# Performance work log

Hardware: AMD Instinct MI355X
Metric: run time of the kernel (lower is better)

## Reference

```python
import jax, jax.numpy as jnp
from jax import lax
import numpy as np

B, T, D = 8, 2048, 1024
EPS = 1e-8


def zc_rms(x, g):
    x0 = x - jnp.mean(x, axis=-1, keepdims=True)
    return x0 * jax.lax.rsqrt(jnp.mean(x0 * x0, axis=-1, keepdims=True) + EPS) * g


def l2norm(x):
    return x * jax.lax.rsqrt(jnp.sum(x * x, axis=-1, keepdims=True) + EPS)


def dwconv3(x, w, b):
    # x: [B, T, D]; w: [D, 3] depthwise kernel; b: [D]
    xc = jnp.transpose(x, (0, 2, 1))  # [B, D, T]
    y = lax.conv_general_dilated(xc, w[:, None, :], window_strides=(1,),
                                 padding=[(1, 1)],
                                 dimension_numbers=('NCH', 'OIH', 'NCH'),
                                 feature_group_count=w.shape[0])
    return jnp.transpose(y + b[:, None], (0, 2, 1))  # [B, T, D]


def setup_inputs() -> dict:
    key = jax.random.key(0)
    ks = jax.random.split(key, 16)
    s = 1.0 / np.sqrt(D)
    inp = {
        'x': jax.random.normal(ks[0], (B, T, D), jnp.float32),
        'g1': jnp.ones((D,), jnp.float32),
        'Wq': jax.random.normal(ks[1], (D, D), jnp.float32) * s,
        'bq': jnp.zeros((D,), jnp.float32),
        'Wk': jax.random.normal(ks[2], (D, D), jnp.float32) * s,
        'bk': jnp.zeros((D,), jnp.float32),
        'Wv': jax.random.normal(ks[3], (D, D), jnp.float32) * s,
        'bv': jnp.zeros((D,), jnp.float32),
        'wqc': jax.random.normal(ks[4], (D, 3), jnp.float32) * 0.5,
        'bqc': jnp.zeros((D,), jnp.float32),
        'wkc': jax.random.normal(ks[5], (D, 3), jnp.float32) * 0.5,
        'bkc': jnp.zeros((D,), jnp.float32),
        'wvc': jax.random.normal(ks[6], (D, 3), jnp.float32) * 0.5,
        'bvc': jnp.zeros((D,), jnp.float32),
        'Wa': jax.random.normal(ks[7], (D, D), jnp.float32) * s,
        'ba': jnp.zeros((D,), jnp.float32),
        'Wb': jax.random.normal(ks[8], (D, D), jnp.float32) * s,
        'bb': jnp.zeros((D,), jnp.float32),
        'g2': jnp.ones((D,), jnp.float32),
        'Wp': jax.random.normal(ks[9], (D, D), jnp.float32) * s,
        'bp': jnp.zeros((D,), jnp.float32),
    }
    return inp


def reference(x, g1, Wq, bq, Wk, bk, Wv, bv, wqc, bqc, wkc, bkc, wvc, bvc,
              Wa, ba, Wb, bb, g2, Wp, bp):
    h = zc_rms(x, g1)
    q = jax.nn.sigmoid(dwconv3(h @ Wq + bq, wqc, bqc))
    k = jax.nn.sigmoid(dwconv3(h @ Wk + bk, wkc, bkc))
    v = jax.nn.sigmoid(dwconv3(h @ Wv + bv, wvc, bvc))
    q, k = l2norm(q), l2norm(k)
    delta = q * (k * v)
    delta = jnp.tanh(x @ Wa + ba) * delta + (x @ Wb + bb)
    dhat = zc_rms(delta, g2) @ Wp + bp
    # dropout is identity in eval mode
    return x + jax.nn.sigmoid(jax.nn.silu(dhat)) * dhat
```

## Files before the change

kernel.cpp:

```cpp
#include <hip/hip_runtime.h>
#include <stdint.h>

#define DD 1024
#define TT 2048
#define BBATCH 8
#define MM (BBATCH*TT)

typedef unsigned short u16;
typedef unsigned int   u32;

typedef __attribute__((ext_vector_type(8))) __bf16 bf16x8;
typedef __attribute__((ext_vector_type(4))) float  floatx4;
typedef __attribute__((ext_vector_type(4))) unsigned short u16x4;
typedef __attribute__((ext_vector_type(8))) unsigned short u16x8;
typedef __attribute__((ext_vector_type(4))) unsigned int   u32x4;

__device__ __forceinline__ float b2f(u16 v){
    u32 x = ((u32)v) << 16;
    return __builtin_bit_cast(float, x);
}
__device__ __forceinline__ u16 f2b(float f){
    u32 u = __builtin_bit_cast(u32, f);
    u32 r = (u + 0x7fffu + ((u >> 16) & 1u)) >> 16;
    return (u16)r;
}
__device__ __forceinline__ float sigf(float x){
    return 1.0f / (1.0f + __expf(-x));
}
__device__ __forceinline__ float tanhfast(float x){
    float e = __expf(2.0f * x);
    return 1.0f - 2.0f / (e + 1.0f);
}

__device__ __forceinline__ void g2l16(const u16* g, u16* l){
    __builtin_amdgcn_global_load_lds(
        (const __attribute__((address_space(1))) u32*)g,
        (__attribute__((address_space(3))) u32*)l, 16, 0, 0);
}

__device__ __forceinline__ u32 lds_u32(const u16* p){
    return (u32)(size_t)(const __attribute__((address_space(3))) u16*)p;
}

template<int OFF>
__device__ __forceinline__ bf16x8 dsr(u32 addr){
    u32x4 d;
    asm volatile("ds_read_b128 %0, %1 offset:%2" : "=v"(d) : "v"(addr), "i"(OFF));
    return __builtin_bit_cast(bf16x8, d);
}

template<int BASE>
__device__ __forceinline__ void rd_a8(bf16x8 (&arr)[8], u32 a0, u32 a1){
    arr[0]=dsr<BASE+0>(a0);    arr[1]=dsr<BASE+0>(a1);
    arr[2]=dsr<BASE+2048>(a0); arr[3]=dsr<BASE+2048>(a1);
    arr[4]=dsr<BASE+4096>(a0); arr[5]=dsr<BASE+4096>(a1);
    arr[6]=dsr<BASE+6144>(a0); arr[7]=dsr<BASE+6144>(a1);
}
template<int BASE>
__device__ __forceinline__ void rd_b4(bf16x8 (&arr)[4], u32 a0, u32 a1){
    arr[0]=dsr<BASE+0>(a0);    arr[1]=dsr<BASE+0>(a1);
    arr[2]=dsr<BASE+2048>(a0); arr[3]=dsr<BASE+2048>(a1);
}

__device__ __forceinline__ void load4bf(const u16* p, float* o){
    u16x4 v = *(const u16x4*)p;
    o[0] = b2f(v.x); o[1] = b2f(v.y); o[2] = b2f(v.z); o[3] = b2f(v.w);
}

__device__ __forceinline__ void wave_reduce2(float& a, float& b){
    #pragma unroll
    for (int m = 32; m; m >>= 1){
        a += __shfl_xor(a, m, 64);
        b += __shfl_xor(b, m, 64);
    }
}

__device__ __forceinline__ void block_reduce2(float& a, float& b, float* red, int tid){
    #pragma unroll
    for (int off = 32; off; off >>= 1){
        a += __shfl_down(a, off, 64);
        b += __shfl_down(b, off, 64);
    }
    __syncthreads();
    if ((tid & 63) == 0){ red[tid >> 6] = a; red[4 + (tid >> 6)] = b; }
    __syncthreads();
    a = red[0] + red[1] + red[2] + red[3];
    b = red[4] + red[5] + red[6] + red[7];
}

__global__ __launch_bounds__(256) void transpose_w(
    const float* __restrict__ s0, const float* __restrict__ s1, const float* __restrict__ s2,
    const float* __restrict__ s3, const float* __restrict__ s4, const float* __restrict__ s5,
    u16* __restrict__ dst_base)
{
    __shared__ u16 tile[32][33];
    const float* srcs[6] = {s0, s1, s2, s3, s4, s5};
    const int z = blockIdx.z;
    const float* src = srcs[z];
    u16* dst = dst_base + (size_t)z * (DD * (size_t)DD);
    const int tx = threadIdx.x, ty = threadIdx.y;
    const int x = blockIdx.x * 32 + tx;
    #pragma unroll
    for (int i = 0; i < 4; i++){
        int y = blockIdx.y * 32 + ty + i * 8;
        tile[ty + i * 8][tx] = f2b(src[(size_t)y * DD + x]);
    }
    __syncthreads();
    const int x2 = blockIdx.y * 32 + tx;
    #pragma unroll
    for (int i = 0; i < 4; i++){
        int y2 = blockIdx.x * 32 + ty + i * 8;
        dst[(size_t)y2 * DD + x2] = tile[tx][ty + i * 8];
    }
}

__global__ __launch_bounds__(256) void prep_wc(
    const float* __restrict__ w0, const float* __restrict__ w1, const float* __restrict__ w2,
    float* __restrict__ wcT)
{
    const float* srcs[3] = {w0, w1, w2};
    const int s = blockIdx.x / 3, tap = blockIdx.x % 3;
    #pragma unroll
    for (int i = 0; i < 4; i++){
        int d = threadIdx.x + i * 256;
        wcT[(s * 3 + tap) * DD + d] = srcs[s][d * 3 + tap];
    }
}

__global__ __launch_bounds__(256) void prep_rows(
    const float* __restrict__ in, const float* __restrict__ g,
    u16* __restrict__ xb, u16* __restrict__ h)
{
    const int tid = threadIdx.x;
    const int w = tid >> 6, lane = tid & 63;
    const int row = blockIdx.x * 4 + w;
    const int d0 = lane * 16;
    const size_t base = (size_t)row * DD + d0;

    float v[16];
    #pragma unroll
    for (int c = 0; c < 4; c++){
        floatx4 t = *(const floatx4*)(in + base + c * 4);
        v[c*4+0] = t.x; v[c*4+1] = t.y; v[c*4+2] = t.z; v[c*4+3] = t.w;
    }
    u16x8 x0, x1;
    #pragma unroll
    for (int j = 0; j < 8; j++){ x0[j] = f2b(v[j]); x1[j] = f2b(v[8+j]); }
    *(u16x8*)(xb + base)     = x0;
    *(u16x8*)(xb + base + 8) = x1;

    float s1 = 0.f, s2 = 0.f;
    #pragma unroll
    for (int j = 0; j < 16; j++){ s1 += v[j]; s2 += v[j]*v[j]; }
    wave_reduce2(s1, s2);
    const float mu = s1 * (1.0f / DD);
    const float ms = fmaxf(s2 * (1.0f / DD) - mu * mu, 0.0f);
    const float sc = rsqrtf(ms + 1e-8f);

    u16x8 o0, o1;
    #pragma unroll
    for (int j = 0; j < 8; j++)  o0[j] = f2b((v[j]     - mu) * sc * g[d0 + j]);
    #pragma unroll
    for (int j = 0; j < 8; j++)  o1[j] = f2b((v[8 + j] - mu) * sc * g[d0 + 8 + j]);
    *(u16x8*)(h + base)     = o0;
    *(u16x8*)(h + base + 8) = o1;
}

struct GemmPtrs {
    const u16*   A[5];
    const u16*   W[5];
    const float* bias[5];
    u16*         out[5];
};

#define BAR()   asm volatile("s_barrier" ::: "memory")
#define LGKM0() asm volatile("s_waitcnt lgkmcnt(0)" ::: "memory")
#define VM4()   asm volatile("s_waitcnt vmcnt(4)" ::: "memory")
#define SB0()   __builtin_amdgcn_sched_barrier(0)
#define PRIO1() __builtin_amdgcn_s_setprio(1)
#define PRIO0() __builtin_amdgcn_s_setprio(0)

template<int IH, int JH>
__device__ __forceinline__ void mm8(floatx4 (&acc)[8][4], const bf16x8 (&af)[8], const bf16x8 (&bf)[4]){
    #pragma unroll
    for (int kk = 0; kk < 2; kk++)
        #pragma unroll
        for (int i = 0; i < 4; i++)
            #pragma unroll
            for (int j = 0; j < 2; j++)
                acc[IH*4+i][JH*2+j] = __builtin_amdgcn_mfma_f32_16x16x32_bf16(
                    af[i*2+kk], bf[j*2+kk], acc[IH*4+i][JH*2+j], 0, 0, 0);
}

template<int MODE>
__global__ __launch_bounds__(512, 2) void gemm_bf16(
    GemmPtrs ptrs, const float* __restrict__ xres, float* __restrict__ dout)
{
    __shared__ alignas(16) u16 lds[65536];

    const int z = blockIdx.z;
    const u16*   __restrict__ A    = ptrs.A[z];
    const u16*   __restrict__ W    = ptrs.W[z];
    const float* __restrict__ bias = ptrs.bias[z];
    u16* __restrict__ Cout = ptrs.out[z];

    const int tid  = threadIdx.x;
    const int wave = tid >> 6, lane = tid & 63;
    const int quad = lane >> 4, l16 = lane & 15;
    const int wrow = wave >> 2, wcol = wave & 3;
    const int bm = blockIdx.x * 256;
    const int bn = blockIdx.y * 256;

    const int coloff = (((tid & 7) ^ ((tid >> 3) & 7)) * 8);
    const u16* srcA = A + (size_t)(bm + (tid >> 3)) * DD + coloff;
    const u16* srcB = W + (size_t)(bn + (tid >> 3)) * DD + coloff;

    #define STAGE_A(T,H) do{ \
        u16* _d = &lds[(((T)&1)*2 + (H))*8192 + tid*8]; \
        const u16* _g = srcA + (size_t)(H)*128*DD + (size_t)(((T)&15)*64); \
        g2l16(_g, _d); g2l16(_g + (size_t)64*DD, _d + 4096); }while(0)
    #define STAGE_B(T,H) do{ \
        u16* _d = &lds[32768 + (((T)&1)*2 + (H))*8192 + tid*8]; \
        const u16* _g = srcB + (size_t)(H)*128*DD + (size_t)(((T)&15)*64); \
        g2l16(_g, _d); g2l16(_g + (size_t)64*DD, _d + 4096); }while(0)

    const u32 lbase = lds_u32(&lds[0]);
    const u32 rowb  = (u32)(l16 * 128);
    const u32 sw0   = (u32)(((quad    ) ^ (l16 & 7)) << 4);
    const u32 sw1   = (u32)(((quad + 4) ^ (l16 & 7)) << 4);
    u32 addr_a0 = lbase + (u32)(wrow * 8192) + rowb + sw0;
    u32 addr_a1 = lbase + (u32)(wrow * 8192) + rowb + sw1;
    u32 addr_b0 = lbase + 65536u + (u32)(wcol * 4096) + rowb + sw0;
    u32 addr_b1 = lbase + 65536u + (u32)(wcol * 4096) + rowb + sw1;

    floatx4 acc[8][4];
    #pragma unroll
    for (int i = 0; i < 8; i++)
        #pragma unroll
        for (int j = 0; j < 4; j++)
            acc[i][j] = (floatx4){0.f, 0.f, 0.f, 0.f};

    STAGE_A(0,0); STAGE_B(0,0); STAGE_B(0,1); STAGE_A(0,1); STAGE_A(1,0); STAGE_B(1,0);
    VM4(); BAR();
    bf16x8 af0[8], af1[8], bf0[4], bf1[4];
    rd_a8<0>(af0, addr_a0, addr_a1);
    rd_b4<0>(bf0, addr_b0, addr_b1);

    for (int t = 0; t < 16; ++t){
        STAGE_B(t+1, 1);
        BAR();
        LGKM0(); SB0();
        PRIO1(); mm8<0,0>(acc, af0, bf0); PRIO0(); SB0();
        rd_b4<16384>(bf1, addr_b0, addr_b1);
        STAGE_A(t+1, 1);
        LGKM0(); SB0();
        PRIO1(); mm8<0,1>(acc, af0, bf1); PRIO0(); SB0();
        rd_a8<16384>(af1, addr_a0, addr_a1);
        VM4(); BAR();
        STAGE_A(t+2, 0);
        BAR();
        LGKM0(); SB0();
        PRIO1(); mm8<1,0>(acc, af1, bf0); PRIO0(); SB0();
        rd_a8<0>(af0, addr_a0 ^ 32768u, addr_a1 ^ 32768u);
        rd_b4<0>(bf0, addr_b0 ^ 32768u, addr_b1 ^ 32768u);
        STAGE_B(t+2, 0);
        PRIO1(); mm8<1,1>(acc, af1, bf1); PRIO0(); SB0();
        VM4(); BAR();
        addr_a0 ^= 32768u; addr_a1 ^= 32768u;
        addr_b0 ^= 32768u; addr_b1 ^= 32768u;
    }
    asm volatile("s_waitcnt vmcnt(0) lgkmcnt(0)" ::: "memory");

    #undef STAGE_A
    #undef STAGE_B

    float bj[4];
    #pragma unroll
    for (int j = 0; j < 4; j++)
        bj[j] = bias[bn + (j >= 2 ? 128 : 0) + wcol * 32 + (j & 1) * 16 + l16];

    #pragma unroll
    for (int i = 0; i < 8; i++){
        const int row0 = bm + (i >= 4 ? 128 : 0) + wrow * 64 + (i & 3) * 16 + quad * 4;
        #pragma unroll
        for (int j = 0; j < 4; j++){
            const int col = bn + (j >= 2 ? 128 : 0) + wcol * 32 + (j & 1) * 16 + l16;
            #pragma unroll
            for (int r = 0; r < 4; r++){
                size_t idx = (size_t)(row0 + r) * DD + col;
                float zv = acc[i][j][r] + bj[j];
                if (MODE == 0){
                    Cout[idx] = f2b(zv);
                } else {
                    float sl = zv * sigf(zv);
                    dout[idx] = xres[idx] + sigf(sl) * zv;
                }
            }
        }
    }
}

__global__ __launch_bounds__(256) void mid_fuse(
    const u16* __restrict__ q0, const u16* __restrict__ k0, const u16* __restrict__ v0,
    const u16* __restrict__ a0, const u16* __restrict__ b0,
    const float* __restrict__ wcT,
    const float* __restrict__ bqc, const float* __restrict__ bkc, const float* __restrict__ bvc,
    const float* __restrict__ g2, u16* __restrict__ uout)
{
    __shared__ float red[8];
    const int bid = blockIdx.x;
    const int row = ((bid & 7) << 11) | (bid >> 3);
    const int t   = row & (TT - 1);
    const int tid = threadIdx.x;
    const int d0  = tid * 4;
    const size_t base = (size_t)row * DD + d0;
    const bool hm = (t > 0), hp = (t < TT - 1);

    float q[4], k[4], v[4];
    {
        const u16*   srcs[3] = {q0, k0, v0};
        const float* bs[3]   = {bqc, bkc, bvc};
        float* outs[3]       = {q, k, v};
        #pragma unroll
        for (int s = 0; s < 3; s++){
            float cm[4], cc[4], cp[4];
            load4bf(srcs[s] + base, cc);
            if (hm) load4bf(srcs[s] + base - DD, cm);
            else { cm[0]=0.f; cm[1]=0.f; cm[2]=0.f; cm[3]=0.f; }
            if (hp) load4bf(srcs[s] + base + DD, cp);
            else { cp[0]=0.f; cp[1]=0.f; cp[2]=0.f; cp[3]=0.f; }
            const float* wt = wcT + s * 3 * DD + d0;
            const float* bb = bs[s] + d0;
            #pragma unroll
            for (int j = 0; j < 4; j++){
                float y = cm[j] * wt[j] + cc[j] * wt[DD + j] + cp[j] * wt[2 * DD + j] + bb[j];
                outs[s][j] = sigf(y);
            }
        }
    }

    float sq = 0.f, sk = 0.f;
    #pragma unroll
    for (int j = 0; j < 4; j++){ sq += q[j] * q[j]; sk += k[j] * k[j]; }
    block_reduce2(sq, sk, red, tid);
    const float rq = rsqrtf(sq + 1e-8f), rk = rsqrtf(sk + 1e-8f);

    float av[4], bv[4];
    load4bf(a0 + base, av);
    load4bf(b0 + base, bv);

    float dl[4], s1 = 0.f, s2 = 0.f;
    #pragma unroll
    for (int j = 0; j < 4; j++){
        float d = (q[j] * rq) * (k[j] * rk) * v[j];
        d = tanhfast(av[j]) * d + bv[j];
        dl[j] = d; s1 += d; s2 += d * d;
    }
    block_reduce2(s1, s2, red, tid);
    const float mu = s1 * (1.0f / DD);
    const float ms = fmaxf(s2 * (1.0f / DD) - mu * mu, 0.0f);
    const float sc = rsqrtf(ms + 1e-8f);

    u16x4 ov;
    ov.x = f2b((dl[0] - mu) * sc * g2[d0 + 0]);
    ov.y = f2b((dl[1] - mu) * sc * g2[d0 + 1]);
    ov.z = f2b((dl[2] - mu) * sc * g2[d0 + 2]);
    ov.w = f2b((dl[3] - mu) * sc * g2[d0 + 3]);
    *(u16x4*)(uout + base) = ov;
}

extern "C" void kernel_launch(void* const* d_in, const int* in_sizes, int n_in,
                              void* d_out, int out_size, void* d_ws, size_t ws_size,
                              hipStream_t stream)
{
    const float* x   = (const float*)d_in[0];
    const float* g1  = (const float*)d_in[1];
    const float* Wq  = (const float*)d_in[2];
    const float* bq  = (const float*)d_in[3];
    const float* Wk  = (const float*)d_in[4];
    const float* bk  = (const float*)d_in[5];
    const float* Wv  = (const float*)d_in[6];
    const float* bv  = (const float*)d_in[7];
    const float* wqc = (const float*)d_in[8];
    const float* bqc = (const float*)d_in[9];
    const float* wkc = (const float*)d_in[10];
    const float* bkc = (const float*)d_in[11];
    const float* wvc = (const float*)d_in[12];
    const float* bvc = (const float*)d_in[13];
    const float* Wa  = (const float*)d_in[14];
    const float* ba  = (const float*)d_in[15];
    const float* Wb  = (const float*)d_in[16];
    const float* bb  = (const float*)d_in[17];
    const float* g2  = (const float*)d_in[18];
    const float* Wp  = (const float*)d_in[19];
    const float* bp  = (const float*)d_in[20];

    u16* ws = (u16*)d_ws;
    const size_t WSZ = (size_t)DD * DD;
    const size_t TSZ = (size_t)MM * DD;
    u16* WT = ws;
    float* wcT = (float*)(ws + 6 * WSZ);
    u16* xb = ws + 6 * WSZ + 32768;
    u16* h  = xb + TSZ;
    u16* q0 = h  + TSZ;
    u16* k0 = q0 + TSZ;
    u16* v0 = k0 + TSZ;
    u16* a0 = v0 + TSZ;
    u16* b0 = a0 + TSZ;
    u16* u  = h;

    transpose_w<<<dim3(32, 32, 6), dim3(32, 8, 1), 0, stream>>>(Wq, Wk, Wv, Wa, Wb, Wp, WT);
    prep_wc<<<dim3(9), dim3(256), 0, stream>>>(wqc, wkc, wvc, wcT);
    prep_rows<<<dim3(MM / 4), dim3(256), 0, stream>>>(x, g1, xb, h);

    GemmPtrs p0;
    p0.A[0] = h;  p0.W[0] = WT + 0 * WSZ; p0.bias[0] = bq; p0.out[0] = q0;
    p0.A[1] = h;  p0.W[1] = WT + 1 * WSZ; p0.bias[1] = bk; p0.out[1] = k0;
    p0.A[2] = h;  p0.W[2] = WT + 2 * WSZ; p0.bias[2] = bv; p0.out[2] = v0;
    p0.A[3] = xb; p0.W[3] = WT + 3 * WSZ; p0.bias[3] = ba; p0.out[3] = a0;
    p0.A[4] = xb; p0.W[4] = WT + 4 * WSZ; p0.bias[4] = bb; p0.out[4] = b0;
    gemm_bf16<0><<<dim3(64, 4, 5), dim3(512), 0, stream>>>(p0, nullptr, nullptr);

    mid_fuse<<<dim3(MM), dim3(256), 0, stream>>>(q0, k0, v0, a0, b0,
                                                 wcT, bqc, bkc, bvc, g2, u);

    GemmPtrs p1;
    for (int i = 0; i < 5; i++){ p1.A[i] = u; p1.W[i] = WT + 5 * WSZ; p1.bias[i] = bp; p1.out[i] = nullptr; }
    gemm_bf16<1><<<dim3(64, 4, 1), dim3(512), 0, stream>>>(p1, x, (float*)d_out);
}
```

Measured before the change: 460.9 us.

## Merge prep kernels and process eight rows per mid_fuse block with window reuse

The three prep kernels (weight transpose, conv-weight reorder, row normalisation) become one launch that dispatches on block index. mid_fuse now handles eight consecutive rows per block, keeping a sliding window of q/k/v neighbour rows in registers. It also holds conv weights, biases and g2 in registers, and prefetches the next row's data. The two block reductions per row are folded into one seven-value reduction by expanding the second normalisation's mean and variance algebraically. This cuts redundant neighbour loads, launches and barriers, but raises register pressure, lowers block count, and the expanded variance formula may be slightly less numerically stable.

```diff
diff --git a/kernel.cpp b/kernel.cpp
--- a/kernel.cpp
+++ b/kernel.cpp
@@ -75,72 +75,79 @@
     }
 }
 
-__device__ __forceinline__ void block_reduce2(float& a, float& b, float* red, int tid){
+__device__ __forceinline__ void block_reduce7(float* v, float* red, int tid){
     #pragma unroll
     for (int off = 32; off; off >>= 1){
-        a += __shfl_down(a, off, 64);
-        b += __shfl_down(b, off, 64);
+        #pragma unroll
+        for (int i = 0; i < 7; i++)
+            v[i] += __shfl_down(v[i], off, 64);
     }
     __syncthreads();
-    if ((tid & 63) == 0){ red[tid >> 6] = a; red[4 + (tid >> 6)] = b; }
+    if ((tid & 63) == 0){
+        #pragma unroll
+        for (int i = 0; i < 7; i++) red[(tid >> 6) * 8 + i] = v[i];
+    }
     __syncthreads();
-    a = red[0] + red[1] + red[2] + red[3];
-    b = red[4] + red[5] + red[6] + red[7];
-}
-
-__global__ __launch_bounds__(256) void transpose_w(
+    #pragma unroll
+    for (int i = 0; i < 7; i++)
+        v[i] = red[i] + red[8 + i] + red[16 + i] + red[24 + i];
+}
+
+__global__ __launch_bounds__(256) void prep_all(
     const float* __restrict__ s0, const float* __restrict__ s1, const float* __restrict__ s2,
     const float* __restrict__ s3, const float* __restrict__ s4, const float* __restrict__ s5,
-    u16* __restrict__ dst_base)
+    u16* __restrict__ WT,
+    const float* __restrict__ w0, const float* __restrict__ w1, const float* __restrict__ w2,
+    float* __restrict__ wcT,
+    const float* __restrict__ x, const float* __restrict__ g1,
+    u16* __restrict__ xb, u16* __restrict__ h)
 {
     __shared__ u16 tile[32][33];
-    const float* srcs[6] = {s0, s1, s2, s3, s4, s5};
-    const int z = blockIdx.z;
-    const float* src = srcs[z];
-    u16* dst = dst_base + (size_t)z * (DD * (size_t)DD);
-    const int tx = threadIdx.x, ty = threadIdx.y;
-    const int x = blockIdx.x * 32 + tx;
-    #pragma unroll
-    for (int i = 0; i < 4; i++){
-        int y = blockIdx.y * 32 + ty + i * 8;
-        tile[ty + i * 8][tx] = f2b(src[(size_t)y * DD + x]);
-    }
-    __syncthreads();
-    const int x2 = blockIdx.y * 32 + tx;
-    #pragma unroll
-    for (int i = 0; i < 4; i++){
-        int y2 = blockIdx.x * 32 + ty + i * 8;
-        dst[(size_t)y2 * DD + x2] = tile[tx][ty + i * 8];
-    }
-}
-
-__global__ __launch_bounds__(256) void prep_wc(
-    const float* __restrict__ w0, const float* __restrict__ w1, const float* __restrict__ w2,
-    float* __restrict__ wcT)
-{
-    const float* srcs[3] = {w0, w1, w2};
-    const int s = blockIdx.x / 3, tap = blockIdx.x % 3;
-    #pragma unroll
-    for (int i = 0; i < 4; i++){
-        int d = threadIdx.x + i * 256;
-        wcT[(s * 3 + tap) * DD + d] = srcs[s][d * 3 + tap];
-    }
-}
-
-__global__ __launch_bounds__(256) void prep_rows(
-    const float* __restrict__ in, const float* __restrict__ g,
-    u16* __restrict__ xb, u16* __restrict__ h)
-{
+    const int bid = blockIdx.x;
     const int tid = threadIdx.x;
+
+    if (bid < 6144){
+        const float* srcs[6] = {s0, s1, s2, s3, s4, s5};
+        const int z  = bid >> 10;
+        const int bi = bid & 1023;
+        const int bx = bi & 31, by = bi >> 5;
+        const float* src = srcs[z];
+        u16* dst = WT + (size_t)z * (DD * (size_t)DD);
+        const int tx = tid & 31, ty = tid >> 5;
+        #pragma unroll
+        for (int i = 0; i < 4; i++){
+            int y = by * 32 + ty + i * 8;
+            tile[ty + i * 8][tx] = f2b(src[(size_t)y * DD + bx * 32 + tx]);
+        }
+        __syncthreads();
+        #pragma unroll
+        for (int i = 0; i < 4; i++){
+            int y2 = bx * 32 + ty + i * 8;
+            dst[(size_t)y2 * DD + by * 32 + tx] = tile[tx][ty + i * 8];
+        }
+        return;
+    }
+    if (bid < 6153){
+        const float* srcs[3] = {w0, w1, w2};
+        const int b = bid - 6144;
+        const int s = b / 3, tap = b % 3;
+        #pragma unroll
+        for (int i = 0; i < 4; i++){
+            int d = tid + i * 256;
+            wcT[(s * 3 + tap) * DD + d] = srcs[s][d * 3 + tap];
+        }
+        return;
+    }
+
     const int w = tid >> 6, lane = tid & 63;
-    const int row = blockIdx.x * 4 + w;
+    const int row = (bid - 6153) * 4 + w;
     const int d0 = lane * 16;
     const size_t base = (size_t)row * DD + d0;
 
     float v[16];
     #pragma unroll
     for (int c = 0; c < 4; c++){
-        floatx4 t = *(const floatx4*)(in + base + c * 4);
+        floatx4 t = *(const floatx4*)(x + base + c * 4);
         v[c*4+0] = t.x; v[c*4+1] = t.y; v[c*4+2] = t.z; v[c*4+3] = t.w;
     }
     u16x8 x0, x1;
@@ -149,19 +156,19 @@
     *(u16x8*)(xb + base)     = x0;
     *(u16x8*)(xb + base + 8) = x1;
 
-    float s1 = 0.f, s2 = 0.f;
-    #pragma unroll
-    for (int j = 0; j < 16; j++){ s1 += v[j]; s2 += v[j]*v[j]; }
-    wave_reduce2(s1, s2);
-    const float mu = s1 * (1.0f / DD);
-    const float ms = fmaxf(s2 * (1.0f / DD) - mu * mu, 0.0f);
+    float p1 = 0.f, p2 = 0.f;
+    #pragma unroll
+    for (int j = 0; j < 16; j++){ p1 += v[j]; p2 += v[j]*v[j]; }
+    wave_reduce2(p1, p2);
+    const float mu = p1 * (1.0f / DD);
+    const float ms = fmaxf(p2 * (1.0f / DD) - mu * mu, 0.0f);
     const float sc = rsqrtf(ms + 1e-8f);
 
     u16x8 o0, o1;
     #pragma unroll
-    for (int j = 0; j < 8; j++)  o0[j] = f2b((v[j]     - mu) * sc * g[d0 + j]);
-    #pragma unroll
-    for (int j = 0; j < 8; j++)  o1[j] = f2b((v[8 + j] - mu) * sc * g[d0 + 8 + j]);
+    for (int j = 0; j < 8; j++)  o0[j] = f2b((v[j]     - mu) * sc * g1[d0 + j]);
+    #pragma unroll
+    for (int j = 0; j < 8; j++)  o1[j] = f2b((v[8 + j] - mu) * sc * g1[d0 + 8 + j]);
     *(u16x8*)(h + base)     = o0;
     *(u16x8*)(h + base + 8) = o1;
 }
@@ -307,66 +314,130 @@
     const float* __restrict__ bqc, const float* __restrict__ bkc, const float* __restrict__ bvc,
     const float* __restrict__ g2, u16* __restrict__ uout)
 {
-    __shared__ float red[8];
-    const int bid = blockIdx.x;
-    const int row = ((bid & 7) << 11) | (bid >> 3);
-    const int t   = row & (TT - 1);
+    __shared__ float red[32];
     const int tid = threadIdx.x;
     const int d0  = tid * 4;
-    const size_t base = (size_t)row * DD + d0;
-    const bool hm = (t > 0), hp = (t < TT - 1);
-
-    float q[4], k[4], v[4];
-    {
-        const u16*   srcs[3] = {q0, k0, v0};
-        const float* bs[3]   = {bqc, bkc, bvc};
-        float* outs[3]       = {q, k, v};
+    const int r0  = blockIdx.x * 8;
+    const int t0  = r0 & (TT - 1);
+    const u16* srcs[3] = {q0, k0, v0};
+    const float* bsrc[3] = {bqc, bkc, bvc};
+
+    float wt[3][3][4], cb[3][4], gv[4];
+    #pragma unroll
+    for (int s = 0; s < 3; s++){
+        #pragma unroll
+        for (int p = 0; p < 3; p++){
+            const float* wp = wcT + (s * 3 + p) * DD + d0;
+            #pragma unroll
+            for (int j = 0; j < 4; j++) wt[s][p][j] = wp[j];
+        }
+        #pragma unroll
+        for (int j = 0; j < 4; j++) cb[s][j] = bsrc[s][d0 + j];
+    }
+    #pragma unroll
+    for (int j = 0; j < 4; j++) gv[j] = g2[d0 + j];
+
+    const size_t base = (size_t)r0 * DD + d0;
+
+    float cm[3][4], cc[3][4], cp[3][4], av[4], bv[4];
+    #pragma unroll
+    for (int s = 0; s < 3; s++){
+        if (t0 > 0) load4bf(srcs[s] + base - DD, cm[s]);
+        else { cm[s][0]=0.f; cm[s][1]=0.f; cm[s][2]=0.f; cm[s][3]=0.f; }
+        load4bf(srcs[s] + base,      cc[s]);
+        load4bf(srcs[s] + base + DD, cp[s]);
+    }
+    load4bf(a0 + base, av);
+    load4bf(b0 + base, bv);
+
+    #pragma unroll
+    for (int r = 0; r < 8; r++){
+        const size_t rb = base + (size_t)r * DD;
+
+        float q[4], k[4], v[4];
+        float* outs[3] = {q, k, v};
         #pragma unroll
         for (int s = 0; s < 3; s++){
-            float cm[4], cc[4], cp[4];
-            load4bf(srcs[s] + base, cc);
-            if (hm) load4bf(srcs[s] + base - DD, cm);
-            else { cm[0]=0.f; cm[1]=0.f; cm[2]=0.f; cm[3]=0.f; }
-            if (hp) load4bf(srcs[s] + base + DD, cp);
-            else { cp[0]=0.f; cp[1]=0.f; cp[2]=0.f; cp[3]=0.f; }
-            const float* wt = wcT + s * 3 * DD + d0;
-            const float* bb = bs[s] + d0;
             #pragma unroll
             for (int j = 0; j < 4; j++){
-                float y = cm[j] * wt[j] + cc[j] * wt[DD + j] + cp[j] * wt[2 * DD + j] + bb[j];
+                float y = cm[s][j] * wt[s][0][j] + cc[s][j] * wt[s][1][j]
+                        + cp[s][j] * wt[s][2][j] + cb[s][j];
                 outs[s][j] = sigf(y);
             }
         }
-    }
-
-    float sq = 0.f, sk = 0.f;
-    #pragma unroll
-    for (int j = 0; j < 4; j++){ sq += q[j] * q[j]; sk += k[j] * k[j]; }
-    block_reduce2(sq, sk, red, tid);
-    const float rq = rsqrtf(sq + 1e-8f), rk = rsqrtf(sk + 1e-8f);
-
-    float av[4], bv[4];
-    load4bf(a0 + base, av);
-    load4bf(b0 + base, bv);
-
-    float dl[4], s1 = 0.f, s2 = 0.f;
-    #pragma unroll
-    for (int j = 0; j < 4; j++){
-        float d = (q[j] * rq) * (k[j] * rk) * v[j];
-        d = tanhfast(av[j]) * d + bv[j];
-        dl[j] = d; s1 += d; s2 += d * d;
-    }
-    block_reduce2(s1, s2, red, tid);
-    const float mu = s1 * (1.0f / DD);
-    const float ms = fmaxf(s2 * (1.0f / DD) - mu * mu, 0.0f);
-    const float sc = rsqrtf(ms + 1e-8f);
-
-    u16x4 ov;
-    ov.x = f2b((dl[0] - mu) * sc * g2[d0 + 0]);
-    ov.y = f2b((dl[1] - mu) * sc * g2[d0 + 1]);
-    ov.z = f2b((dl[2] - mu) * sc * g2[d0 + 2]);
-    ov.w = f2b((dl[3] - mu) * sc * g2[d0 + 3]);
-    *(u16x4*)(uout + base) = ov;
+
+        float w4[4], p[7];
+        p[0]=0.f; p[1]=0.f; p[2]=0.f; p[3]=0.f; p[4]=0.f; p[5]=0.f; p[6]=0.f;
+        #pragma unroll
+        for (int j = 0; j < 4; j++){
+            float ww = tanhfast(av[j]) * q[j] * k[j] * v[j];
+            w4[j] = ww;
+            p[0] += q[j] * q[j];
+            p[1] += k[j] * k[j];
+            p[2] += ww;
+            p[3] += ww * ww;
+            p[4] += ww * bv[j];
+            p[5] += bv[j];
+            p[6] += bv[j] * bv[j];
+        }
+
+        float cpn[3][4], avn[4], bvn[4];
+        if (r < 7){
+            const size_t nb = rb + DD;
+            const bool hv = (t0 + r + 2) <= (TT - 1);
+            #pragma unroll
+            for (int s = 0; s < 3; s++){
+                if (hv) load4bf(srcs[s] + nb + DD, cpn[s]);
+                else { cpn[s][0]=0.f; cpn[s][1]=0.f; cpn[s][2]=0.f; cpn[s][3]=0.f; }
+            }
+            load4bf(a0 + nb, avn);
+            load4bf(b0 + nb, bvn);
+
+            block_reduce7(p, red, tid);
+
+            const float rq = rsqrtf(p[0] + 1e-8f);
+            const float rk = rsqrtf(p[1] + 1e-8f);
+            const float C  = rq * rk;
+            const float ss1 = C * p[2] + p[5];
+            const float ss2 = C * C * p[3] + 2.0f * C * p[4] + p[6];
+            const float mu = ss1 * (1.0f / DD);
+            const float ms = fmaxf(ss2 * (1.0f / DD) - mu * mu, 0.0f);
+            const float sc = rsqrtf(ms + 1e-8f);
+            u16x4 ov;
+            ov.x = f2b((C * w4[0] + bv[0] - mu) * sc * gv[0]);
+            ov.y = f2b((C * w4[1] + bv[1] - mu) * sc * gv[1]);
+            ov.z = f2b((C * w4[2] + bv[2] - mu) * sc * gv[2]);
+            ov.w = f2b((C * w4[3] + bv[3] - mu) * sc * gv[3]);
+            *(u16x4*)(uout + rb) = ov;
+
+            #pragma unroll
+            for (int s = 0; s < 3; s++){
+                #pragma unroll
+                for (int j = 0; j < 4; j++){
+                    cm[s][j] = cc[s][j]; cc[s][j] = cp[s][j]; cp[s][j] = cpn[s][j];
+                }
+            }
+            #pragma unroll
+            for (int j = 0; j < 4; j++){ av[j] = avn[j]; bv[j] = bvn[j]; }
+        } else {
+            block_reduce7(p, red, tid);
+
+            const float rq = rsqrtf(p[0] + 1e-8f);
+            const float rk = rsqrtf(p[1] + 1e-8f);
+            const float C  = rq * rk;
+            const float ss1 = C * p[2] + p[5];
+            const float ss2 = C * C * p[3] + 2.0f * C * p[4] + p[6];
+            const float mu = ss1 * (1.0f / DD);
+            const float ms = fmaxf(ss2 * (1.0f / DD) - mu * mu, 0.0f);
+            const float sc = rsqrtf(ms + 1e-8f);
+            u16x4 ov;
+            ov.x = f2b((C * w4[0] + bv[0] - mu) * sc * gv[0]);
+            ov.y = f2b((C * w4[1] + bv[1] - mu) * sc * gv[1]);
+            ov.z = f2b((C * w4[2] + bv[2] - mu) * sc * gv[2]);
+            ov.w = f2b((C * w4[3] + bv[3] - mu) * sc * gv[3]);
+            *(u16x4*)(uout + rb) = ov;
+        }
+    }
 }
 
 extern "C" void kernel_launch(void* const* d_in, const int* in_sizes, int n_in,
@@ -409,9 +480,8 @@
     u16* b0 = a0 + TSZ;
     u16* u  = h;
 
-    transpose_w<<<dim3(32, 32, 6), dim3(32, 8, 1), 0, stream>>>(Wq, Wk, Wv, Wa, Wb, Wp, WT);
-    prep_wc<<<dim3(9), dim3(256), 0, stream>>>(wqc, wkc, wvc, wcT);
-    prep_rows<<<dim3(MM / 4), dim3(256), 0, stream>>>(x, g1, xb, h);
+    prep_all<<<dim3(10249), dim3(256), 0, stream>>>(
+        Wq, Wk, Wv, Wa, Wb, Wp, WT, wqc, wkc, wvc, wcT, x, g1, xb, h);
 
     GemmPtrs p0;
     p0.A[0] = h;  p0.W[0] = WT + 0 * WSZ; p0.bias[0] = bq; p0.out[0] = q0;
@@ -421,8 +491,8 @@
     p0.A[4] = xb; p0.W[4] = WT + 4 * WSZ; p0.bias[4] = bb; p0.out[4] = b0;
     gemm_bf16<0><<<dim3(64, 4, 5), dim3(512), 0, stream>>>(p0, nullptr, nullptr);
 
-    mid_fuse<<<dim3(MM), dim3(256), 0, stream>>>(q0, k0, v0, a0, b0,
-                                                 wcT, bqc, bkc, bvc, g2, u);
+    mid_fuse<<<dim3(MM / 8), dim3(256), 0, stream>>>(q0, k0, v0, a0, b0,
+                                                     wcT, bqc, bkc, bvc, g2, u);
 
     GemmPtrs p1;
     for (int i = 0; i < 5; i++){ p1.A[i] = u; p1.W[i] = WT + 5 * WSZ; p1.bias[i] = bp; p1.out[i] = nullptr; }
```

New measurement: 448.3 us. 2.7% less time.
